# Optimization experiments

Hardware: AMD Instinct MI355X
Metric: run time of the kernel (lower is better)

The kernel has to match this reference:

```python
import jax, jax.numpy as jnp
import numpy as np

E = 200      # word2vec_embed_size
D = 768      # hidden_size
LN_EPS = 1e-12


def setup_inputs() -> dict:
    key = jax.random.key(0)
    ks = jax.random.split(key, 9)
    B, L, W = 16, 512, 8
    std = 0.02
    return {
        "word_embeddings": jax.random.normal(ks[0], (B, L, W, E), jnp.float32),
        "layer_output": jax.random.normal(ks[1], (B, L, D), jnp.float32),
        "Wt": jax.random.normal(ks[2], (D, E), jnp.float32) * std,   # word_transform weight
        "bt": jnp.zeros((D,), jnp.float32),
        "Ww": jax.random.normal(ks[3], (D, D), jnp.float32) * std,   # word_word_weight weight
        "bw": jnp.zeros((D,), jnp.float32),
        "attn_W": jax.random.normal(ks[4], (D, D), jnp.float32) * std,
        "ln_gamma": jnp.ones((D,), jnp.float32),
        "ln_beta": jnp.zeros((D,), jnp.float32),
    }


def _layernorm(x, gamma, beta):
    mu = jnp.mean(x, axis=-1, keepdims=True)
    var = jnp.mean(jnp.square(x - mu), axis=-1, keepdims=True)
    return (x - mu) * jax.lax.rsqrt(var + LN_EPS) * gamma + beta


def reference(word_embeddings, layer_output, Wt, bt, Ww, bw, attn_W, ln_gamma, ln_beta):
    # word_transform -> tanh -> word_word_weight   (dropout = identity in eval)
    wo = jnp.tanh(jnp.einsum('blwe,de->blwd', word_embeddings, Wt) + bt)
    wo = jnp.einsum('blwd,ed->blwe', wo, Ww) + bw          # [B,L,W,D]
    # bilinear char-word attention: (layer @ attn_W) . wo over D
    q = jnp.einsum('bld,de->ble', layer_output, attn_W)    # [B,L,D]
    alpha = jnp.einsum('bld,blwd->blw', q, wo)             # [B,L,W]
    alpha = jax.nn.softmax(alpha, axis=-1)
    weighted = jnp.einsum('blw,blwd->bld', alpha, wo)      # [B,L,D]
    fused = layer_output + weighted                        # residual (dropout = identity)
    return _layernorm(fused, ln_gamma, ln_beta)
```

## Files before the change

kernel.cpp:

```cpp
#include <hip/hip_runtime.h>
#include <hip/hip_bf16.h>


typedef __bf16 bf16_t;
typedef bf16_t bf16x4 __attribute__((ext_vector_type(4)));
typedef bf16_t bf16x8 __attribute__((ext_vector_type(8)));
typedef float f32x4 __attribute__((ext_vector_type(4)));

__device__ __forceinline__ bf16x4 cvt4(float4 v) {
  bf16x4 o;
  o[0] = (bf16_t)v.x; o[1] = (bf16_t)v.y;
  o[2] = (bf16_t)v.z; o[3] = (bf16_t)v.w;
  return o;
}

__global__ void prep_wt(const float* __restrict__ Wt, bf16_t* __restrict__ Wtb) {
  const int u = blockIdx.x * 256 + threadIdx.x;
  const int lane = u & 63;
  const int v = u >> 6;
  const int kt = v % 7;
  const int v2 = v / 7;
  const int jg = v2 & 7, nt = v2 >> 3;
  const int l16 = lane & 15, quad = lane >> 4;
  const int n = nt * 128 + jg * 16 + l16;
  const int k0 = kt * 32 + quad * 8;
  float4 a = {0.f, 0.f, 0.f, 0.f}, b = {0.f, 0.f, 0.f, 0.f};
  if (k0 < 200) {
    a = *(const float4*)(Wt + n * 200 + k0);
    b = *(const float4*)(Wt + n * 200 + k0 + 4);
  }
  *(bf16x4*)&Wtb[u * 8] = cvt4(a);
  *(bf16x4*)&Wtb[u * 8 + 4] = cvt4(b);
}

__global__ void prep_ww(const float* __restrict__ Ww, bf16_t* __restrict__ Wwf) {
  const int u = blockIdx.x * 256 + threadIdx.x;
  const int lane = u & 63;
  const int v = u >> 6;
  const int kt = v % 24;
  const int jg = v / 24;
  const int l16 = lane & 15, quad = lane >> 4;
  const long n = jg * 16 + l16;
  const int k0 = kt * 32 + quad * 8;
  float4 a = *(const float4*)(Ww + n * 768 + k0);
  float4 b = *(const float4*)(Ww + n * 768 + k0 + 4);
  *(bf16x4*)&Wwf[u * 8] = cvt4(a);
  *(bf16x4*)&Wwf[u * 8 + 4] = cvt4(b);
}

__global__ __launch_bounds__(256, 2) void gemm_nn(
    const float* __restrict__ A, const float* __restrict__ B,
    float* __restrict__ C, int ldA, int ldB, int N_out, int kFull) {
  __shared__ __align__(16) bf16_t As[128 * 32];
  __shared__ __align__(16) bf16_t Bs[32 * 128];

  const int t = threadIdx.x;
  const int lane = t & 63, wave = t >> 6;
  const int wr = wave >> 1, wc = wave & 1;
  const int quad = lane >> 4, l16 = lane & 15;
  const long m0 = (long)blockIdx.y * 128;
  const long n0 = (long)blockIdx.x * 128;

  f32x4 acc[4][4] = {};

  for (int kt = 0; kt < kFull; ++kt) {
    const int k0 = kt * 32;
#pragma unroll
    for (int r = 0; r < 4; ++r) {
      const int f = r * 256 + t;
      const int arow = f >> 3, ak = (f & 7) * 4;
      float4 va = *(const float4*)(A + (m0 + arow) * ldA + k0 + ak);
      *(bf16x4*)&As[arow * 32 + ak] = cvt4(va);
      const int brow = f >> 5, bc = (f & 31) * 4;
      float4 vb = *(const float4*)(B + (long)(k0 + brow) * ldB + n0 + bc);
      *(bf16x4*)&Bs[brow * 128 + bc] = cvt4(vb);
    }
    __syncthreads();

    bf16x8 af[4], bfv[4];
#pragma unroll
    for (int i = 0; i < 4; ++i)
      af[i] = *(const bf16x8*)&As[(wr * 64 + i * 16 + l16) * 32 + quad * 8];
#pragma unroll
    for (int j = 0; j < 4; ++j) {
      const int n = wc * 64 + j * 16 + l16;
#pragma unroll
      for (int jj = 0; jj < 8; ++jj)
        bfv[j][jj] = Bs[(quad * 8 + jj) * 128 + n];
    }
#pragma unroll
    for (int i = 0; i < 4; ++i)
#pragma unroll
      for (int j = 0; j < 4; ++j)
        acc[i][j] = __builtin_amdgcn_mfma_f32_16x16x32_bf16(af[i], bfv[j],
                                                            acc[i][j], 0, 0, 0);
    __syncthreads();
  }

#pragma unroll
  for (int j = 0; j < 4; ++j) {
    const long n = n0 + wc * 64 + j * 16 + l16;
#pragma unroll
    for (int i = 0; i < 4; ++i) {
      const long mBase = m0 + wr * 64 + i * 16 + quad * 4;
#pragma unroll
      for (int r = 0; r < 4; ++r)
        C[(mBase + r) * N_out + n] = acc[i][j][r];
    }
  }
}

#define ASF_LD 232
__global__ __launch_bounds__(256, 2) void x1_attn(
    const float* __restrict__ WE, const bf16_t* __restrict__ Wtb,
    const float* __restrict__ bt, const float* __restrict__ R,
    bf16_t* __restrict__ Yb) {
  __shared__ __align__(16) bf16_t As[64 * ASF_LD];
  __shared__ float red[8][8][2];
  __shared__ float alphaS[8][8];

  const int t = threadIdx.x;
  const int lane = t & 63, wave = t >> 6;
  const int wr = wave >> 1, wc = wave & 1;
  const int quad = lane >> 4, l16 = lane & 15;
  const int ghalf = quad >> 1, wq = (quad & 1) * 4;
  const long m0 = (long)blockIdx.x * 64;
  const long gbase = (long)blockIdx.x * 8;

  const float* WEb = WE + m0 * 200;
#pragma unroll
  for (int r = 0; r < 13; ++r) {
    const int f = r * 256 + t;
    if (f < 3200) {
      const int row = f / 50, idx = f - row * 50;
      *(bf16x4*)&As[row * ASF_LD + idx * 4] =
          cvt4(*(const float4*)(WEb + 4 * f));
    }
  }
  {
    const bf16x4 z4 = {(bf16_t)0.f, (bf16_t)0.f, (bf16_t)0.f, (bf16_t)0.f};
#pragma unroll
    for (int p = 0; p < 2; ++p) {
      const int s = p * 256 + t;
      *(bf16x4*)&As[(s >> 3) * ASF_LD + 200 + (s & 7) * 4] = z4;
    }
  }
  __syncthreads();

  bf16x4 st[6][2][4];
  float pl[2][4] = {};

#pragma unroll
  for (int nt = 0; nt < 6; ++nt) {
    f32x4 acc[2][4] = {};
    const bf16_t* bb = Wtb + ((nt * 8 + wc * 4) * 7) * 512 + lane * 8;
#pragma unroll
    for (int kt = 0; kt < 7; ++kt) {
      bf16x8 af[2], bf[4];
#pragma unroll
      for (int i = 0; i < 2; ++i)
        af[i] = *(const bf16x8*)&As[(wr * 32 + i * 16 + l16) * ASF_LD +
                                    kt * 32 + quad * 8];
#pragma unroll
      for (int j = 0; j < 4; ++j)
        bf[j] = *(const bf16x8*)&bb[(j * 7 + kt) * 512];
#pragma unroll
      for (int i = 0; i < 2; ++i)
#pragma unroll
        for (int j = 0; j < 4; ++j)
          acc[i][j] = __builtin_amdgcn_mfma_f32_16x16x32_bf16(
              af[i], bf[j], acc[i][j], 0, 0, 0);
    }
    const int nb = nt * 128 + wc * 64;
#pragma unroll
    for (int j = 0; j < 4; ++j) {
      const int n = nb + j * 16 + l16;
      const float btv = bt[n];
#pragma unroll
      for (int i = 0; i < 2; ++i) {
        const long grow = gbase + 4 * wr + 2 * i + ghalf;
        const float Rv = R[grow * 768 + n];
#pragma unroll
        for (int r = 0; r < 4; ++r) {
          const float vv = acc[i][j][r] + btv;
          const float e = __expf(2.f * vv);
          const float x = 1.f - __fdividef(2.f, e + 1.f);
          st[nt][i][j][r] = (bf16_t)x;
          pl[i][r] += x * Rv;
        }
      }
    }
  }

#pragma unroll
  for (int o = 8; o > 0; o >>= 1)
#pragma unroll
    for (int i = 0; i < 2; ++i)
#pragma unroll
      for (int r = 0; r < 4; ++r)
        pl[i][r] += __shfl_down(pl[i][r], o, 16);
  if (l16 == 0) {
#pragma unroll
    for (int i = 0; i < 2; ++i)
#pragma unroll
      for (int r = 0; r < 4; ++r)
        red[4 * wr + 2 * i + ghalf][wq + r][wc] = pl[i][r];
  }
  __syncthreads();

  if (t < 64) {
    const int g = t >> 3, w = t & 7;
    const float lg = red[g][w][0] + red[g][w][1];
    float mx = lg;
#pragma unroll
    for (int o = 4; o > 0; o >>= 1) mx = fmaxf(mx, __shfl_xor(mx, o, 8));
    const float e = __expf(lg - mx);
    float s = e;
#pragma unroll
    for (int o = 4; o > 0; o >>= 1) s += __shfl_xor(s, o, 8);
    alphaS[g][w] = __fdividef(e, s);
  }
  __syncthreads();

#pragma unroll
  for (int i = 0; i < 2; ++i) {
    const int glo = 4 * wr + 2 * i + ghalf;
    const long grow = gbase + glo;
    const float a0 = alphaS[glo][wq + 0], a1 = alphaS[glo][wq + 1];
    const float a2 = alphaS[glo][wq + 2], a3 = alphaS[glo][wq + 3];
#pragma unroll
    for (int nt = 0; nt < 6; ++nt) {
#pragma unroll
      for (int j = 0; j < 4; ++j) {
        float py = a0 * (float)st[nt][i][j][0] + a1 * (float)st[nt][i][j][1] +
                   a2 * (float)st[nt][i][j][2] + a3 * (float)st[nt][i][j][3];
        py += __shfl_xor(py, 16);
        if ((quad & 1) == 0)
          Yb[grow * 768 + nt * 128 + wc * 64 + j * 16 + l16] = (bf16_t)py;
      }
    }
  }
}

__global__ __launch_bounds__(256, 2) void y_ww_ln(
    const bf16_t* __restrict__ Yb, const bf16_t* __restrict__ Wwf,
    const float* __restrict__ bw, const float* __restrict__ LO,
    const float* __restrict__ gamma, const float* __restrict__ beta,
    float* __restrict__ out) {
  __shared__ float rowstats[32][4][2];

  const int t = threadIdx.x;
  const int lane = t & 63, wc = t >> 6;
  const int quad = lane >> 4, l16 = lane & 15;
  const long m0 = (long)blockIdx.x * 32;

  f32x4 acc[2][12] = {};

#define LD_FRAGS(af_, bf_, kt_)                                               \
  {                                                                           \
    _Pragma("unroll") for (int i_ = 0; i_ < 2; ++i_)                          \
        af_[i_] = *(const bf16x8*)&Yb[(m0 + i_ * 16 + l16) * 768 +            \
                                      (kt_) * 32 + quad * 8];                 \
    _Pragma("unroll") for (int j_ = 0; j_ < 12; ++j_)                         \
        bf_[j_] = *(const bf16x8*)&Wwf[(((wc * 12 + j_) * 24 + (kt_)) << 9) + \
                                       lane * 8];                             \
  }

  bf16x8 afA[2], bfA[12], afB[2], bfB[12];
  LD_FRAGS(afA, bfA, 0);
  for (int kt = 0; kt < 24; kt += 2) {
    LD_FRAGS(afB, bfB, kt + 1);
#pragma unroll
    for (int i = 0; i < 2; ++i)
#pragma unroll
      for (int j = 0; j < 12; ++j)
        acc[i][j] = __builtin_amdgcn_mfma_f32_16x16x32_bf16(afA[i], bfA[j],
                                                            acc[i][j], 0, 0, 0);
    if (kt + 2 < 24) LD_FRAGS(afA, bfA, kt + 2);
#pragma unroll
    for (int i = 0; i < 2; ++i)
#pragma unroll
      for (int j = 0; j < 12; ++j)
        acc[i][j] = __builtin_amdgcn_mfma_f32_16x16x32_bf16(afB[i], bfB[j],
                                                            acc[i][j], 0, 0, 0);
  }
#undef LD_FRAGS

  float s1[2][4] = {}, s2[2][4] = {};
#pragma unroll
  for (int i = 0; i < 2; ++i)
#pragma unroll
    for (int j = 0; j < 12; ++j) {
      const int n = wc * 192 + j * 16 + l16;
      const float bwv = bw[n];
#pragma unroll
      for (int r = 0; r < 4; ++r) {
        const int ml = i * 16 + quad * 4 + r;
        const float fv = acc[i][j][r] + bwv + LO[(m0 + ml) * 768 + n];
        acc[i][j][r] = fv;
        s1[i][r] += fv;
        s2[i][r] += fv * fv;
      }
    }
#pragma unroll
  for (int o = 8; o > 0; o >>= 1)
#pragma unroll
    for (int i = 0; i < 2; ++i)
#pragma unroll
      for (int r = 0; r < 4; ++r) {
        s1[i][r] += __shfl_down(s1[i][r], o, 16);
        s2[i][r] += __shfl_down(s2[i][r], o, 16);
      }
  if (l16 == 0)
#pragma unroll
    for (int i = 0; i < 2; ++i)
#pragma unroll
      for (int r = 0; r < 4; ++r) {
        const int ml = i * 16 + quad * 4 + r;
        rowstats[ml][wc][0] = s1[i][r];
        rowstats[ml][wc][1] = s2[i][r];
      }
  __syncthreads();

#pragma unroll
  for (int i = 0; i < 2; ++i) {
    float mu[4], istd[4];
#pragma unroll
    for (int r = 0; r < 4; ++r) {
      const int ml = i * 16 + quad * 4 + r;
      const float S1 = rowstats[ml][0][0] + rowstats[ml][1][0] +
                       rowstats[ml][2][0] + rowstats[ml][3][0];
      const float S2 = rowstats[ml][0][1] + rowstats[ml][1][1] +
                       rowstats[ml][2][1] + rowstats[ml][3][1];
      mu[r] = S1 * (1.f / 768.f);
      const float var = S2 * (1.f / 768.f) - mu[r] * mu[r];
      istd[r] = rsqrtf(var + 1e-12f);
    }
#pragma unroll
    for (int j = 0; j < 12; ++j) {
      const int n = wc * 192 + j * 16 + l16;
      const float gv = gamma[n], bv = beta[n];
#pragma unroll
      for (int r = 0; r < 4; ++r) {
        const int ml = i * 16 + quad * 4 + r;
        out[(m0 + ml) * 768 + n] = (acc[i][j][r] - mu[r]) * istd[r] * gv + bv;
      }
    }
  }
}

extern "C" void kernel_launch(void* const* d_in, const int* in_sizes, int n_in,
                              void* d_out, int out_size, void* d_ws,
                              size_t ws_size, hipStream_t stream) {
  (void)in_sizes; (void)n_in; (void)out_size; (void)ws_size;
  const float* WE = (const float*)d_in[0];
  const float* LO = (const float*)d_in[1];
  const float* Wt = (const float*)d_in[2];
  const float* bt = (const float*)d_in[3];
  const float* Ww = (const float*)d_in[4];
  const float* bw = (const float*)d_in[5];
  const float* aW = (const float*)d_in[6];
  const float* g  = (const float*)d_in[7];
  const float* bb = (const float*)d_in[8];
  float* out = (float*)d_out;

  char* ws = (char*)d_ws;
  const size_t WC_BYTES  = (size_t)768 * 768 * 4;
  const size_t WTB_BYTES = (size_t)6 * 8 * 7 * 64 * 8 * 2;
  const size_t WWF_BYTES = (size_t)48 * 24 * 64 * 8 * 2;
  float*  Wc  = (float*)ws;
  bf16_t* Wtb = (bf16_t*)(ws + WC_BYTES);
  bf16_t* Wwf = (bf16_t*)(ws + WC_BYTES + WTB_BYTES);
  bf16_t* Yb  = (bf16_t*)(ws + WC_BYTES + WTB_BYTES + WWF_BYTES);

  const dim3 blk(256);

  prep_wt<<<dim3(84), blk, 0, stream>>>(Wt, Wtb);
  prep_ww<<<dim3(288), blk, 0, stream>>>(Ww, Wwf);
  gemm_nn<<<dim3(6, 6), blk, 0, stream>>>(aW, Ww, Wc, 768, 768, 768, 24);
  gemm_nn<<<dim3(6, 64), blk, 0, stream>>>(LO, Wc, out, 768, 768, 768, 24);
  x1_attn<<<dim3(1024), blk, 0, stream>>>(WE, Wtb, bt, out, Yb);
  y_ww_ln<<<dim3(256), blk, 0, stream>>>(Yb, Wwf, bw, LO, g, bb, out);
}
```

Before: 305.0 us.

## Retile GEMMs into 1024-thread blocks with register prefetch; halve attention tile

Replaces the generic LDS-tiled gemm for R=LO·Wc with a new register-prefetched MFMA kernel that reads a pre-swizzled bf16 copy of Wc, made by a new prep kernel. The attention kernel now handles 32 rows per block instead of 64, which doubles the grid, raises the occupancy hint, adds double-buffered weight fragments, and stages Y in LDS for a coalesced store. The Ww+LayerNorm kernel moves to 1024-thread blocks with 16 waves per 32 rows and a two-stage row-stats reduction. The aim is more parallelism and better latency hiding, at the cost of an extra launch and more redundant A-fragment loads across waves.

```diff
diff --git a/kernel.cpp b/kernel.cpp
--- a/kernel.cpp
+++ b/kernel.cpp
@@ -12,6 +12,12 @@
   o[0] = (bf16_t)v.x; o[1] = (bf16_t)v.y;
   o[2] = (bf16_t)v.z; o[3] = (bf16_t)v.w;
   return o;
+}
+__device__ __forceinline__ bf16x8 cvt8(float4 a, float4 b) {
+  bf16x8 v;
+  v[0] = (bf16_t)a.x; v[1] = (bf16_t)a.y; v[2] = (bf16_t)a.z; v[3] = (bf16_t)a.w;
+  v[4] = (bf16_t)b.x; v[5] = (bf16_t)b.y; v[6] = (bf16_t)b.z; v[7] = (bf16_t)b.w;
+  return v;
 }
 
 __global__ void prep_wt(const float* __restrict__ Wt, bf16_t* __restrict__ Wtb) {
@@ -48,6 +54,21 @@
   *(bf16x4*)&Wwf[u * 8 + 4] = cvt4(b);
 }
 
+__global__ void prep_wc(const float* __restrict__ Wc, bf16_t* __restrict__ Wcf) {
+  const int u = blockIdx.x * 256 + threadIdx.x;
+  const int lane = u & 63;
+  const int v = u >> 6;
+  const int kt = v % 24;
+  const int jg = v / 24;
+  const int l16 = lane & 15, quad = lane >> 4;
+  const int n = jg * 16 + l16;
+  const int k0 = kt * 32 + quad * 8;
+  bf16x8 o;
+#pragma unroll
+  for (int e = 0; e < 8; ++e) o[e] = (bf16_t)Wc[(long)(k0 + e) * 768 + n];
+  *(bf16x8*)&Wcf[u * 8] = o;
+}
+
 __global__ __launch_bounds__(256, 2) void gemm_nn(
     const float* __restrict__ A, const float* __restrict__ B,
     float* __restrict__ C, int ldA, int ldB, int N_out, int kFull) {
@@ -110,28 +131,89 @@
   }
 }
 
+__global__ __launch_bounds__(1024, 4) void gemm_r(
+    const float* __restrict__ LO, const bf16_t* __restrict__ Wcf,
+    float* __restrict__ Rout) {
+  const int t = threadIdx.x;
+  const int lane = t & 63, w = t >> 6;
+  const int quad = lane >> 4, l16 = lane & 15;
+  const long m0 = (long)blockIdx.x * 32;
+
+  const float* a0p = LO + (m0 + l16) * 768 + quad * 8;
+  const float* a1p = LO + (m0 + 16 + l16) * 768 + quad * 8;
+  const bf16_t* bp = Wcf + ((size_t)(w * 3) * 24 << 9) + lane * 8;
+
+  f32x4 acc[2][3] = {};
+  bf16x8 afC[2], afP[2], bfC[3], bfP[3];
+
+#define LDA_R(dst, kt_)                                                  \
+  {                                                                      \
+    dst[0] = cvt8(*(const float4*)(a0p + (kt_) * 32),                    \
+                  *(const float4*)(a0p + (kt_) * 32 + 4));               \
+    dst[1] = cvt8(*(const float4*)(a1p + (kt_) * 32),                    \
+                  *(const float4*)(a1p + (kt_) * 32 + 4));               \
+  }
+#define LDB_R(dst, kt_)                                                  \
+  {                                                                      \
+    _Pragma("unroll") for (int j_ = 0; j_ < 3; ++j_)                     \
+        dst[j_] = *(const bf16x8*)(bp + ((j_ * 24 + (kt_)) << 9));       \
+  }
+
+  LDA_R(afC, 0); LDB_R(bfC, 0);
+#pragma unroll
+  for (int kt = 0; kt < 24; ++kt) {
+    if (kt < 23) { LDA_R(afP, kt + 1); LDB_R(bfP, kt + 1); }
+#pragma unroll
+    for (int i = 0; i < 2; ++i)
+#pragma unroll
+      for (int j = 0; j < 3; ++j)
+        acc[i][j] = __builtin_amdgcn_mfma_f32_16x16x32_bf16(afC[i], bfC[j],
+                                                            acc[i][j], 0, 0, 0);
+    if (kt < 23) {
+#pragma unroll
+      for (int i = 0; i < 2; ++i) afC[i] = afP[i];
+#pragma unroll
+      for (int j = 0; j < 3; ++j) bfC[j] = bfP[j];
+    }
+  }
+#undef LDA_R
+#undef LDB_R
+
+#pragma unroll
+  for (int i = 0; i < 2; ++i)
+#pragma unroll
+    for (int j = 0; j < 3; ++j) {
+      const int n = w * 48 + j * 16 + l16;
+#pragma unroll
+      for (int r = 0; r < 4; ++r) {
+        const int ml = i * 16 + quad * 4 + r;
+        Rout[(m0 + ml) * 768 + n] = acc[i][j][r];
+      }
+    }
+}
+
 #define ASF_LD 232
-__global__ __launch_bounds__(256, 2) void x1_attn(
+__global__ __launch_bounds__(256, 4) void x1_attn(
     const float* __restrict__ WE, const bf16_t* __restrict__ Wtb,
     const float* __restrict__ bt, const float* __restrict__ R,
     bf16_t* __restrict__ Yb) {
-  __shared__ __align__(16) bf16_t As[64 * ASF_LD];
-  __shared__ float red[8][8][2];
-  __shared__ float alphaS[8][8];
+  __shared__ __align__(16) bf16_t As[32 * ASF_LD];
+  __shared__ __align__(16) bf16_t Ybuf[4 * 768];
+  __shared__ float red[4][8][4];
+  __shared__ float alphaS[4][8];
 
   const int t = threadIdx.x;
-  const int lane = t & 63, wave = t >> 6;
-  const int wr = wave >> 1, wc = wave & 1;
+  const int lane = t & 63, wc = t >> 6;
   const int quad = lane >> 4, l16 = lane & 15;
   const int ghalf = quad >> 1, wq = (quad & 1) * 4;
-  const long m0 = (long)blockIdx.x * 64;
-  const long gbase = (long)blockIdx.x * 8;
+  const long m0 = (long)blockIdx.x * 32;
+  const long gbase = (long)blockIdx.x * 4;
 
   const float* WEb = WE + m0 * 200;
 #pragma unroll
-  for (int r = 0; r < 13; ++r) {
+  for (int r = 0; r < 7; ++r) {
     const int f = r * 256 + t;
-    if (f < 3200) {
+    if (f < 1600) {
       const int row = f / 50, idx = f - row * 50;
       *(bf16x4*)&As[row * ASF_LD + idx * 4] =
           cvt4(*(const float4*)(WEb + 4 * f));
@@ -139,47 +221,48 @@
   }
   {
     const bf16x4 z4 = {(bf16_t)0.f, (bf16_t)0.f, (bf16_t)0.f, (bf16_t)0.f};
-#pragma unroll
-    for (int p = 0; p < 2; ++p) {
-      const int s = p * 256 + t;
-      *(bf16x4*)&As[(s >> 3) * ASF_LD + 200 + (s & 7) * 4] = z4;
-    }
-  }
-  __syncthreads();
-
-  bf16x4 st[6][2][4];
+    *(bf16x4*)&As[(t >> 3) * ASF_LD + 200 + (t & 7) * 4] = z4;
+  }
+  __syncthreads();
+
+  bf16x4 st[6][2][2];
   float pl[2][4] = {};
 
+  const bf16_t* bbase = Wtb + (size_t)lane * 8;
+
+  bf16x8 bfC0 = *(const bf16x8*)(bbase + (size_t)(((wc * 2 + 0) * 7) << 9));
+  bf16x8 bfC1 = *(const bf16x8*)(bbase + (size_t)(((wc * 2 + 1) * 7) << 9));
+  bf16x8 bfP0, bfP1;
+
 #pragma unroll
   for (int nt = 0; nt < 6; ++nt) {
-    f32x4 acc[2][4] = {};
-    const bf16_t* bb = Wtb + ((nt * 8 + wc * 4) * 7) * 512 + lane * 8;
+    f32x4 acc[2][2] = {};
 #pragma unroll
     for (int kt = 0; kt < 7; ++kt) {
-      bf16x8 af[2], bf[4];
-#pragma unroll
-      for (int i = 0; i < 2; ++i)
-        af[i] = *(const bf16x8*)&As[(wr * 32 + i * 16 + l16) * ASF_LD +
-                                    kt * 32 + quad * 8];
-#pragma unroll
-      for (int j = 0; j < 4; ++j)
-        bf[j] = *(const bf16x8*)&bb[(j * 7 + kt) * 512];
-#pragma unroll
-      for (int i = 0; i < 2; ++i)
-#pragma unroll
-        for (int j = 0; j < 4; ++j)
-          acc[i][j] = __builtin_amdgcn_mfma_f32_16x16x32_bf16(
-              af[i], bf[j], acc[i][j], 0, 0, 0);
-    }
-    const int nb = nt * 128 + wc * 64;
-#pragma unroll
-    for (int j = 0; j < 4; ++j) {
+      if (!(nt == 5 && kt == 6)) {
+        const int nnt = (kt == 6) ? nt + 1 : nt;
+        const int nkt = (kt == 6) ? 0 : kt + 1;
+        bfP0 = *(const bf16x8*)(bbase +
+                                (size_t)(((nnt * 8 + wc * 2 + 0) * 7 + nkt) << 9));
+        bfP1 = *(const bf16x8*)(bbase +
+                                (size_t)(((nnt * 8 + wc * 2 + 1) * 7 + nkt) << 9));
+      }
+      bf16x8 af0 = *(const bf16x8*)&As[l16 * ASF_LD + kt * 32 + quad * 8];
+      bf16x8 af1 = *(const bf16x8*)&As[(16 + l16) * ASF_LD + kt * 32 + quad * 8];
+      acc[0][0] = __builtin_amdgcn_mfma_f32_16x16x32_bf16(af0, bfC0, acc[0][0], 0, 0, 0);
+      acc[0][1] = __builtin_amdgcn_mfma_f32_16x16x32_bf16(af0, bfC1, acc[0][1], 0, 0, 0);
+      acc[1][0] = __builtin_amdgcn_mfma_f32_16x16x32_bf16(af1, bfC0, acc[1][0], 0, 0, 0);
+      acc[1][1] = __builtin_amdgcn_mfma_f32_16x16x32_bf16(af1, bfC1, acc[1][1], 0, 0, 0);
+      bfC0 = bfP0; bfC1 = bfP1;
+    }
+    const int nb = nt * 128 + wc * 32;
+#pragma unroll
+    for (int j = 0; j < 2; ++j) {
       const int n = nb + j * 16 + l16;
       const float btv = bt[n];
 #pragma unroll
       for (int i = 0; i < 2; ++i) {
-        const long grow = gbase + 4 * wr + 2 * i + ghalf;
-        const float Rv = R[grow * 768 + n];
+        const float Rv = R[(gbase + i * 2 + ghalf) * 768 + n];
 #pragma unroll
         for (int r = 0; r < 4; ++r) {
           const float vv = acc[i][j][r] + btv;
@@ -199,18 +282,17 @@
 #pragma unroll
       for (int r = 0; r < 4; ++r)
         pl[i][r] += __shfl_down(pl[i][r], o, 16);
-  if (l16 == 0) {
+  if (l16 == 0)
 #pragma unroll
     for (int i = 0; i < 2; ++i)
 #pragma unroll
       for (int r = 0; r < 4; ++r)
-        red[4 * wr + 2 * i + ghalf][wq + r][wc] = pl[i][r];
-  }
-  __syncthreads();
-
-  if (t < 64) {
-    const int g = t >> 3, w = t & 7;
-    const float lg = red[g][w][0] + red[g][w][1];
+        red[i * 2 + ghalf][wq + r][wc] = pl[i][r];
+  __syncthreads();
+
+  if (t < 32) {
+    const int g = t >> 3, w8 = t & 7;
+    const float lg = red[g][w8][0] + red[g][w8][1] + red[g][w8][2] + red[g][w8][3];
     float mx = lg;
 #pragma unroll
     for (int o = 4; o > 0; o >>= 1) mx = fmaxf(mx, __shfl_xor(mx, o, 8));
@@ -218,80 +300,92 @@
     float s = e;
 #pragma unroll
     for (int o = 4; o > 0; o >>= 1) s += __shfl_xor(s, o, 8);
-    alphaS[g][w] = __fdividef(e, s);
+    alphaS[g][w8] = __fdividef(e, s);
   }
   __syncthreads();
 
 #pragma unroll
   for (int i = 0; i < 2; ++i) {
-    const int glo = 4 * wr + 2 * i + ghalf;
-    const long grow = gbase + glo;
+    const int glo = i * 2 + ghalf;
     const float a0 = alphaS[glo][wq + 0], a1 = alphaS[glo][wq + 1];
     const float a2 = alphaS[glo][wq + 2], a3 = alphaS[glo][wq + 3];
 #pragma unroll
-    for (int nt = 0; nt < 6; ++nt) {
-#pragma unroll
-      for (int j = 0; j < 4; ++j) {
+    for (int nt = 0; nt < 6; ++nt)
+#pragma unroll
+      for (int j = 0; j < 2; ++j) {
         float py = a0 * (float)st[nt][i][j][0] + a1 * (float)st[nt][i][j][1] +
                    a2 * (float)st[nt][i][j][2] + a3 * (float)st[nt][i][j][3];
         py += __shfl_xor(py, 16);
         if ((quad & 1) == 0)
-          Yb[grow * 768 + nt * 128 + wc * 64 + j * 16 + l16] = (bf16_t)py;
-      }
-    }
-  }
-}
-
-__global__ __launch_bounds__(256, 2) void y_ww_ln(
+          Ybuf[glo * 768 + nt * 128 + wc * 32 + j * 16 + l16] = (bf16_t)py;
+      }
+  }
+  __syncthreads();
+  {
+    const float4* src = (const float4*)Ybuf;
+    float4* dst = (float4*)(Yb + gbase * 768);
+    dst[t] = src[t];
+    if (t < 128) dst[256 + t] = src[256 + t];
+  }
+}
+
+__global__ __launch_bounds__(1024, 4) void y_ww_ln(
     const bf16_t* __restrict__ Yb, const bf16_t* __restrict__ Wwf,
     const float* __restrict__ bw, const float* __restrict__ LO,
     const float* __restrict__ gamma, const float* __restrict__ beta,
     float* __restrict__ out) {
-  __shared__ float rowstats[32][4][2];
+  __shared__ float rowstats[16][32][2];
+  __shared__ float mustd[32][2];
 
   const int t = threadIdx.x;
-  const int lane = t & 63, wc = t >> 6;
+  const int lane = t & 63, w = t >> 6;
   const int quad = lane >> 4, l16 = lane & 15;
   const long m0 = (long)blockIdx.x * 32;
 
-  f32x4 acc[2][12] = {};
-
-#define LD_FRAGS(af_, bf_, kt_)                                               \
-  {                                                                           \
-    _Pragma("unroll") for (int i_ = 0; i_ < 2; ++i_)                          \
-        af_[i_] = *(const bf16x8*)&Yb[(m0 + i_ * 16 + l16) * 768 +            \
-                                      (kt_) * 32 + quad * 8];                 \
-    _Pragma("unroll") for (int j_ = 0; j_ < 12; ++j_)                         \
-        bf_[j_] = *(const bf16x8*)&Wwf[(((wc * 12 + j_) * 24 + (kt_)) << 9) + \
-                                       lane * 8];                             \
-  }
-
-  bf16x8 afA[2], bfA[12], afB[2], bfB[12];
-  LD_FRAGS(afA, bfA, 0);
-  for (int kt = 0; kt < 24; kt += 2) {
-    LD_FRAGS(afB, bfB, kt + 1);
-#pragma unroll
-    for (int i = 0; i < 2; ++i)
-#pragma unroll
-      for (int j = 0; j < 12; ++j)
-        acc[i][j] = __builtin_amdgcn_mfma_f32_16x16x32_bf16(afA[i], bfA[j],
+  const bf16_t* a0p = Yb + (m0 + l16) * 768 + quad * 8;
+  const bf16_t* a1p = Yb + (m0 + 16 + l16) * 768 + quad * 8;
+  const bf16_t* bp = Wwf + ((size_t)(w * 3) * 24 << 9) + lane * 8;
+
+  f32x4 acc[2][3] = {};
+  bf16x8 afC[2], afP[2], bfC[3], bfP[3];
+
+#define LDA_Y(dst, kt_)                                             \
+  {                                                                 \
+    dst[0] = *(const bf16x8*)(a0p + (kt_) * 32);                    \
+    dst[1] = *(const bf16x8*)(a1p + (kt_) * 32);                    \
+  }
+#define LDB_Y(dst, kt_)                                             \
+  {                                                                 \
+    _Pragma("unroll") for (int j_ = 0; j_ < 3; ++j_)                \
+        dst[j_] = *(const bf16x8*)(bp + ((j_ * 24 + (kt_)) << 9));  \
+  }
+
+  LDA_Y(afC, 0); LDB_Y(bfC, 0);
+#pragma unroll
+  for (int kt = 0; kt < 24; ++kt) {
+    if (kt < 23) { LDA_Y(afP, kt + 1); LDB_Y(bfP, kt + 1); }
+#pragma unroll
+    for (int i = 0; i < 2; ++i)
+#pragma unroll
+      for (int j = 0; j < 3; ++j)
+        acc[i][j] = __builtin_amdgcn_mfma_f32_16x16x32_bf16(afC[i], bfC[j],
                                                             acc[i][j], 0, 0, 0);
-    if (kt + 2 < 24) LD_FRAGS(afA, bfA, kt + 2);
-#pragma unroll
-    for (int i = 0; i < 2; ++i)
-#pragma unroll
-      for (int j = 0; j < 12; ++j)
-        acc[i][j] = __builtin_amdgcn_mfma_f32_16x16x32_bf16(afB[i], bfB[j],
-                                                            acc[i][j], 0, 0, 0);
-  }
-#undef LD_FRAGS
+    if (kt < 23) {
+#pragma unroll
+      for (int i = 0; i < 2; ++i) afC[i] = afP[i];
+#pragma unroll
+      for (int j = 0; j < 3; ++j) bfC[j] = bfP[j];
+    }
+  }
+#undef LDA_Y
+#undef LDB_Y
 
   float s1[2][4] = {}, s2[2][4] = {};
 #pragma unroll
   for (int i = 0; i < 2; ++i)
 #pragma unroll
-    for (int j = 0; j < 12; ++j) {
-      const int n = wc * 192 + j * 16 + l16;
+    for (int j = 0; j < 3; ++j) {
+      const int n = w * 48 + j * 16 + l16;
       const float bwv = bw[n];
 #pragma unroll
       for (int r = 0; r < 4; ++r) {
@@ -317,36 +411,38 @@
 #pragma unroll
       for (int r = 0; r < 4; ++r) {
         const int ml = i * 16 + quad * 4 + r;
-        rowstats[ml][wc][0] = s1[i][r];
-        rowstats[ml][wc][1] = s2[i][r];
-      }
-  __syncthreads();
-
-#pragma unroll
-  for (int i = 0; i < 2; ++i) {
-    float mu[4], istd[4];
-#pragma unroll
-    for (int r = 0; r < 4; ++r) {
-      const int ml = i * 16 + quad * 4 + r;
-      const float S1 = rowstats[ml][0][0] + rowstats[ml][1][0] +
-                       rowstats[ml][2][0] + rowstats[ml][3][0];
-      const float S2 = rowstats[ml][0][1] + rowstats[ml][1][1] +
-                       rowstats[ml][2][1] + rowstats[ml][3][1];
-      mu[r] = S1 * (1.f / 768.f);
-      const float var = S2 * (1.f / 768.f) - mu[r] * mu[r];
-      istd[r] = rsqrtf(var + 1e-12f);
-    }
-#pragma unroll
-    for (int j = 0; j < 12; ++j) {
-      const int n = wc * 192 + j * 16 + l16;
+        rowstats[w][ml][0] = s1[i][r];
+        rowstats[w][ml][1] = s2[i][r];
+      }
+  __syncthreads();
+
+  if (t < 32) {
+    float S1 = 0.f, S2 = 0.f;
+#pragma unroll
+    for (int ww = 0; ww < 16; ++ww) {
+      S1 += rowstats[ww][t][0];
+      S2 += rowstats[ww][t][1];
+    }
+    const float mu = S1 * (1.f / 768.f);
+    const float var = S2 * (1.f / 768.f) - mu * mu;
+    mustd[t][0] = mu;
+    mustd[t][1] = rsqrtf(var + 1e-12f);
+  }
+  __syncthreads();
+
+#pragma unroll
+  for (int i = 0; i < 2; ++i)
+#pragma unroll
+    for (int j = 0; j < 3; ++j) {
+      const int n = w * 48 + j * 16 + l16;
       const float gv = gamma[n], bv = beta[n];
 #pragma unroll
       for (int r = 0; r < 4; ++r) {
         const int ml = i * 16 + quad * 4 + r;
-        out[(m0 + ml) * 768 + n] = (acc[i][j][r] - mu[r]) * istd[r] * gv + bv;
-      }
-    }
-  }
+        out[(m0 + ml) * 768 + n] =
+            (acc[i][j][r] - mustd[ml][0]) * mustd[ml][1] * gv + bv;
+      }
+    }
 }
 
 extern "C" void kernel_launch(void* const* d_in, const int* in_sizes, int n_in,
@@ -368,17 +464,21 @@
   const size_t WC_BYTES  = (size_t)768 * 768 * 4;
   const size_t WTB_BYTES = (size_t)6 * 8 * 7 * 64 * 8 * 2;
   const size_t WWF_BYTES = (size_t)48 * 24 * 64 * 8 * 2;
+  const size_t WCF_BYTES = WWF_BYTES;
   float*  Wc  = (float*)ws;
   bf16_t* Wtb = (bf16_t*)(ws + WC_BYTES);
   bf16_t* Wwf = (bf16_t*)(ws + WC_BYTES + WTB_BYTES);
-  bf16_t* Yb  = (bf16_t*)(ws + WC_BYTES + WTB_BYTES + WWF_BYTES);
+  bf16_t* Wcf = (bf16_t*)(ws + WC_BYTES + WTB_BYTES + WWF_BYTES);
+  bf16_t* Yb  = (bf16_t*)(ws + WC_BYTES + WTB_BYTES + WWF_BYTES + WCF_BYTES);
 
   const dim3 blk(256);
+  const dim3 blk1k(1024);
 
   prep_wt<<<dim3(84), blk, 0, stream>>>(Wt, Wtb);
   prep_ww<<<dim3(288), blk, 0, stream>>>(Ww, Wwf);
   gemm_nn<<<dim3(6, 6), blk, 0, stream>>>(aW, Ww, Wc, 768, 768, 768, 24);
-  gemm_nn<<<dim3(6, 64), blk, 0, stream>>>(LO, Wc, out, 768, 768, 768, 24);
-  x1_attn<<<dim3(1024), blk, 0, stream>>>(WE, Wtb, bt, out, Yb);
-  y_ww_ln<<<dim3(256), blk, 0, stream>>>(Yb, Wwf, bw, LO, g, bb, out);
-}
+  prep_wc<<<dim3(288), blk, 0, stream>>>(Wc, Wcf);
+  gemm_r<<<dim3(256), blk1k, 0, stream>>>(LO, Wcf, out);
+  x1_attn<<<dim3(2048), blk, 0, stream>>>(WE, Wtb, bt, out, Yb);
+  y_ww_ln<<<dim3(256), blk1k, 0, stream>>>(Yb, Wwf, bw, LO, g, bb, out);
+}
```

Measured after the change: 325.0 us. 1.07x slower.
